# Optimization experiments

Measured on AMD Instinct MI355X. Metric: run time of the kernel, lower is better.

The kernel has to match this reference:

```python
import jax, jax.numpy as jnp
import numpy as np

B, CIN, H, W = 8, 64, 128, 128
COUT, K = 64, 3
STRIDE, PAD, DIL, G = 1, 1, 1, 1
T = K * K
HO = (H + 2 * PAD - (DIL * (K - 1) + 1)) // STRIDE + 1
WO = (W + 2 * PAD - (DIL * (K - 1) + 1)) // STRIDE + 1


def setup_inputs() -> dict:
    key = jax.random.key(0)
    ks = jax.random.split(key, 5)
    x = jax.random.normal(ks[0], (B, CIN, H, W), jnp.float32)
    offset = jax.random.normal(ks[1], (B, 2 * G * T, HO, WO), jnp.float32)
    mask = jax.random.uniform(ks[2], (B, G * T, HO, WO), jnp.float32)
    weight = jax.random.normal(ks[3], (COUT, CIN, K, K), jnp.float32) * (1.0 / np.sqrt(CIN * T))
    bias = jnp.zeros((COUT,), jnp.float32)
    return {"x": x, "offset": offset, "mask": mask, "weight": weight, "bias": bias}


def _gather(img_f, idx):
    # img_f: [Cg, H*W], idx: [T, Ho, Wo] -> [Cg, T, Ho, Wo]
    return img_f[:, idx]


def _dcn(x, offset, mask, weight, bias):
    Bn, Cin, Hh, Ww = x.shape
    Cout = weight.shape[0]
    Cg = Cin // G
    # offset channels laid out as [G, T, (dy, dx)] per DCNv2 convention
    off = offset.reshape(Bn, G, T, 2, HO, WO)
    dy, dx = off[:, :, :, 0], off[:, :, :, 1]  # [B, G, T, Ho, Wo]
    ky, kx = jnp.meshgrid(jnp.arange(K), jnp.arange(K), indexing="ij")
    ky = (ky.reshape(T) * DIL).astype(jnp.float32)
    kx = (kx.reshape(T) * DIL).astype(jnp.float32)
    base_y = (jnp.arange(HO) * STRIDE - PAD).astype(jnp.float32)
    base_x = (jnp.arange(WO) * STRIDE - PAD).astype(jnp.float32)
    # absolute sampling coordinates per (batch, def-group, tap, out-row, out-col)
    py = dy + base_y[None, None, None, :, None] + ky[None, None, :, None, None]
    px = dx + base_x[None, None, None, None, :] + kx[None, None, :, None, None]
    y0 = jnp.floor(py)
    x0 = jnp.floor(px)
    imgf = x.reshape(Bn, G, Cg, Hh * Ww)
    gather = jax.vmap(jax.vmap(_gather))  # over B and G
    sampled = jnp.zeros((Bn, G, Cg, T, HO, WO), x.dtype)
    # bilinear interpolation with zero padding outside the image
    for oy, ox in ((y0, x0), (y0, x0 + 1.0), (y0 + 1.0, x0), (y0 + 1.0, x0 + 1.0)):
        wgt = (1.0 - jnp.abs(py - oy)) * (1.0 - jnp.abs(px - ox))
        valid = (oy >= 0) & (oy < Hh) & (ox >= 0) & (ox < Ww)
        yi = jnp.clip(oy, 0, Hh - 1).astype(jnp.int32)
        xi = jnp.clip(ox, 0, Ww - 1).astype(jnp.int32)
        vals = gather(imgf, yi * Ww + xi)  # [B, G, Cg, T, Ho, Wo]
        sampled = sampled + vals * (wgt * valid)[:, :, None]
    # modulation mask, then accumulate taps into output channels
    m = mask.reshape(Bn, G, T, HO, WO)
    sampled = sampled * m[:, :, None]
    wr = weight.reshape(Cout, G, Cg, T)
    out = jnp.einsum("bgctij,ogct->boij", sampled, wr) + bias[None, :, None, None]
    return out


def reference(x, offset, mask, weight, bias):
    return _dcn(x, offset, mask, weight, bias)
```

## Files before the change

### kernel.cpp

```cpp
#include <hip/hip_runtime.h>
#include <stdint.h>

#define Bn   8
#define CIN  64
#define Hh   128
#define Wh   128
#define COUT 64
#define Tt   9
#define HO   128
#define WO   128
#define HW   (HO * WO)

#define RH     17
#define RWC    24
#define RREC   (RH * RWC)
#define HALO_Y 4
#define HALO_X 4

typedef _Float16 h16;
typedef __attribute__((ext_vector_type(2)))  _Float16 h2;
typedef __attribute__((ext_vector_type(8)))  _Float16 h8;
typedef __attribute__((ext_vector_type(16))) float    f16v;

__device__ h16 g_xT[(size_t)Bn * Hh * Wh * CIN];
__device__ h16 g_wh[Tt * 4 * 2 * 64 * 8];

__global__ __launch_bounds__(256) void prep(const float* __restrict__ x,
                                            const float* __restrict__ w) {
    if (blockIdx.x >= Bn * Hh) {
        int tid = (blockIdx.x - Bn * Hh) * 256 + threadIdx.x;
        int t   = tid >> 12;
        int rem = tid & 4095;
        int ks  = rem >> 10;
        int mt  = (rem >> 9) & 1;
        int ln  = (rem >> 3) & 63;
        int j   = rem & 7;
        int o   = mt * 32 + (ln & 31);
        int c   = ks * 16 + ((ln >> 5) << 3) + j;
        g_wh[tid] = (h16)w[(size_t)(o * 64 + c) * 9 + t];
        return;
    }
    int b = blockIdx.x >> 7;
    int y = blockIdx.x & 127;
    __shared__ uint32_t tile[64][65];

    const float* src = x + ((size_t)b * CIN) * (Hh * Wh) + (size_t)y * Wh;
    int t    = threadIdx.x;
    int xp   = t & 63;
    int csub = t >> 6;
    #pragma unroll
    for (int cc = 0; cc < 64; cc += 4) {
        int c = cc + csub;
        float2 v = *(const float2*)(src + (size_t)c * (Hh * Wh) + xp * 2);
        uint32_t h0 = (uint32_t)__builtin_bit_cast(uint16_t, (h16)v.x);
        uint32_t h1 = (uint32_t)__builtin_bit_cast(uint16_t, (h16)v.y);
        tile[c][xp] = h0 | (h1 << 16);
    }
    __syncthreads();

    uint32_t* dst = (uint32_t*)(g_xT + (((size_t)b * Hh + y) * Wh) * CIN);
    int d  = t & 31;
    int xo = t >> 5;
    #pragma unroll
    for (int it = 0; it < 16; ++it) {
        int xg = it * 8 + xo;
        uint32_t lo = tile[2 * d][xg >> 1];
        uint32_t hi = tile[2 * d + 1][xg >> 1];
        int sh = (xg & 1) * 16;
        uint32_t l0 = (lo >> sh) & 0xffffu;
        uint32_t h1 = (hi >> sh) & 0xffffu;
        dst[xg * 32 + d] = l0 | (h1 << 16);
    }
}

__global__ __launch_bounds__(256, 3) void dcn_main(
        const float* __restrict__ offset, const float* __restrict__ mask,
        const float* __restrict__ bias, float* __restrict__ out) {
    __shared__ __align__(16) uint8_t sreg[RREC * 128];

    int blk  = blockIdx.x;
    int b    = blk & 7;
    int s    = blk >> 3;
    int ty   = s >> 3, tx = s & 7;
    int i0   = ty * 8, j0 = tx * 16;
    int lane = threadIdx.x & 63;
    int wave = threadIdx.x >> 6;
    int n    = lane & 31;
    int g    = lane >> 5;

    const h16* xb = g_xT + (size_t)b * (Hh * Wh * CIN);

    int i = i0 + 2 * wave + (n >> 4);
    int j = j0 + (n & 15);
    int p = (i << 7) + j;

    const float* offB = offset + (size_t)b * (2 * Tt * HW);
    const float* mskB = mask   + (size_t)b * (Tt * HW);
    float dyv[Tt], dxv[Tt], mmv[Tt];
    #pragma unroll
    for (int t = 0; t < Tt; ++t) {
        dyv[t] = offB[(2 * t) * HW + p];
        dxv[t] = offB[(2 * t + 1) * HW + p];
        mmv[t] = mskB[t * HW + p];
    }

    {
        const int base_y = i0 - HALO_Y, base_x = j0 - HALO_X;
        #pragma unroll
        for (int it = 0; it < 13; ++it) {
            int idx  = it * 256 + threadIdx.x;
            int rec  = idx >> 3;
            int quad = idx & 7;
            if (rec < RREC) {
                int ry = rec / RWC, rx = rec - ry * RWC;
                int gy = min(max(base_y + ry, 0), Hh - 1);
                int gx = min(max(base_x + rx, 0), Wh - 1);
                uint4 v = *(const uint4*)(xb + ((gy << 7) + gx) * 64 + quad * 8);
                int qs = quad ^ (rec & 7);
                *(uint4*)(sreg + rec * 128 + qs * 16) = v;
            }
        }
    }
    __syncthreads();

    f16v acc[2] = {};

    #pragma unroll
    for (int t = 0; t < Tt; ++t) {
        const int ky = t / 3, kx = t % 3;
        float py = dyv[t] + (float)(i + ky - 1);
        float px = dxv[t] + (float)(j + kx - 1);
        float fy = floorf(py), fx = floorf(px);
        int   y0 = (int)fy,    x0 = (int)fx;
        float ly = py - fy,    lx = px - fx;
        float hy = 1.f - ly,   hx = 1.f - lx;

        bool vy0 = (y0 >= 0) && (y0 < Hh);
        bool vy1 = (y0 >= -1) && (y0 < Hh - 1);
        bool vx0 = (x0 >= 0) && (x0 < Wh);
        bool vx1 = (x0 >= -1) && (x0 < Wh - 1);
        float m = mmv[t];
        float w00 = (vy0 && vx0) ? hy * hx * m : 0.f;
        float w01 = (vy0 && vx1) ? hy * lx * m : 0.f;
        float w10 = (vy1 && vx0) ? ly * hx * m : 0.f;
        float w11 = (vy1 && vx1) ? ly * lx * m : 0.f;

        int ry = y0 - i0 + HALO_Y;
        int rx = x0 - j0 + HALO_X;
        bool intile = (ry >= 0) & (ry <= RH - 2) & (rx >= 0) & (rx <= RWC - 2);
        int ryc = min(max(ry, 0), RH - 2), rxc = min(max(rx, 0), RWC - 2);
        int pl00 = ryc * RWC + rxc;
        int r00 = pl00, r01 = pl00 + 1, r10 = pl00 + RWC, r11 = pl00 + RWC + 1;
        int q00 = ((r00 << 7) | (g << 4)) ^ ((r00 & 7) << 4);
        int q01 = ((r01 << 7) | (g << 4)) ^ ((r01 & 7) << 4);
        int q10 = ((r10 << 7) | (g << 4)) ^ ((r10 & 7) << 4);
        int q11 = ((r11 << 7) | (g << 4)) ^ ((r11 & 7) << 4);

        union U4 { uint4 v; h2 h[4]; };
        U4 c00[4], c01[4], c10[4], c11[4];
        #pragma unroll
        for (int ks = 0; ks < 4; ++ks) {
            c00[ks].v = *(const uint4*)(sreg + (q00 ^ (ks << 5)));
            c01[ks].v = *(const uint4*)(sreg + (q01 ^ (ks << 5)));
            c10[ks].v = *(const uint4*)(sreg + (q10 ^ (ks << 5)));
            c11[ks].v = *(const uint4*)(sreg + (q11 ^ (ks << 5)));
        }
        if (__any(!intile)) {
            if (!intile) {
                int y0c = min(max(y0, 0), Hh - 1), y1c = min(max(y0 + 1, 0), Hh - 1);
                int x0c = min(max(x0, 0), Wh - 1), x1c = min(max(x0 + 1, 0), Wh - 1);
                const h16* r0p = xb + (size_t)(y0c * Wh) * CIN;
                const h16* r1p = xb + (size_t)(y1c * Wh) * CIN;
                #pragma unroll
                for (int ks = 0; ks < 4; ++ks) {
                    int c = ks * 16 + g * 8;
                    c00[ks].v = *(const uint4*)(r0p + x0c * CIN + c);
                    c01[ks].v = *(const uint4*)(r0p + x1c * CIN + c);
                    c10[ks].v = *(const uint4*)(r1p + x0c * CIN + c);
                    c11[ks].v = *(const uint4*)(r1p + x1c * CIN + c);
                }
            }
        }

        h2 W00 = {(h16)w00, (h16)w00};
        h2 W01 = {(h16)w01, (h16)w01};
        h2 W10 = {(h16)w10, (h16)w10};
        h2 W11 = {(h16)w11, (h16)w11};

        const h16* wt = g_wh + t * 4096;
        #pragma unroll
        for (int ks = 0; ks < 4; ++ks) {
            union { h2 r[4]; h8 v; } pk;
            #pragma unroll
            for (int e = 0; e < 4; ++e) {
                h2 r = c00[ks].h[e] * W00;
                r = c01[ks].h[e] * W01 + r;
                r = c10[ks].h[e] * W10 + r;
                r = c11[ks].h[e] * W11 + r;
                pk.r[e] = r;
            }
            #pragma unroll
            for (int mt = 0; mt < 2; ++mt) {
                h8 a = *(const h8*)(wt + (ks * 2 + mt) * 512 + lane * 8);
                acc[mt] = __builtin_amdgcn_mfma_f32_32x32x16_f16(
                    a, pk.v, acc[mt], 0, 0, 0);
            }
        }
    }

    #pragma unroll
    for (int mt = 0; mt < 2; ++mt) {
        #pragma unroll
        for (int r = 0; r < 16; ++r) {
            int o = mt * 32 + (r & 3) + 8 * (r >> 2) + 4 * g;
            out[(size_t)(b * COUT + o) * HW + p] = acc[mt][r] + bias[o];
        }
    }
}

extern "C" void kernel_launch(void* const* d_in, const int* in_sizes, int n_in,
                              void* d_out, int out_size, void* d_ws, size_t ws_size,
                              hipStream_t stream) {
    const float* x      = (const float*)d_in[0];
    const float* offset = (const float*)d_in[1];
    const float* mask   = (const float*)d_in[2];
    const float* weight = (const float*)d_in[3];
    const float* bias   = (const float*)d_in[4];
    (void)d_ws; (void)ws_size;

    prep<<<Bn * Hh + 144, 256, 0, stream>>>(x, weight);
    dcn_main<<<Bn * 128, 256, 0, stream>>>(offset, mask, bias, (float*)d_out);
}
```

Baseline: 120.9 us.

## Process two tiles per block, prefetching second tile's halo into registers during compute

Measured after the change: 140.1 us. 15.9% more time.

```diff
diff --git a/kernel.cpp b/kernel.cpp
--- a/kernel.cpp
+++ b/kernel.cpp
@@ -73,56 +73,55 @@
     }
 }
 
-__global__ __launch_bounds__(256, 3) void dcn_main(
-        const float* __restrict__ offset, const float* __restrict__ mask,
-        const float* __restrict__ bias, float* __restrict__ out) {
-    __shared__ __align__(16) uint8_t sreg[RREC * 128];
-
-    int blk  = blockIdx.x;
-    int b    = blk & 7;
-    int s    = blk >> 3;
-    int ty   = s >> 3, tx = s & 7;
-    int i0   = ty * 8, j0 = tx * 16;
-    int lane = threadIdx.x & 63;
-    int wave = threadIdx.x >> 6;
-    int n    = lane & 31;
-    int g    = lane >> 5;
-
-    const h16* xb = g_xT + (size_t)b * (Hh * Wh * CIN);
-
-    int i = i0 + 2 * wave + (n >> 4);
-    int j = j0 + (n & 15);
-    int p = (i << 7) + j;
-
-    const float* offB = offset + (size_t)b * (2 * Tt * HW);
-    const float* mskB = mask   + (size_t)b * (Tt * HW);
-    float dyv[Tt], dxv[Tt], mmv[Tt];
+
+__device__ __forceinline__ void stage_load(const h16* __restrict__ xb,
+                                           int base_y, int base_x, int tid,
+                                           uint4 sv[13]) {
+    #pragma unroll
+    for (int it = 0; it < 13; ++it) {
+        int idx  = it * 256 + tid;
+        int rec  = idx >> 3;
+        int quad = idx & 7;
+        if (rec < RREC) {
+            int ry = rec / RWC, rx = rec - ry * RWC;
+            int gy = min(max(base_y + ry, 0), Hh - 1);
+            int gx = min(max(base_x + rx, 0), Wh - 1);
+            sv[it] = *(const uint4*)(xb + ((gy << 7) + gx) * 64 + quad * 8);
+        }
+    }
+}
+
+__device__ __forceinline__ void stage_write(uint8_t* __restrict__ sreg,
+                                            int tid, const uint4 sv[13]) {
+    #pragma unroll
+    for (int it = 0; it < 13; ++it) {
+        int idx  = it * 256 + tid;
+        int rec  = idx >> 3;
+        int quad = idx & 7;
+        if (rec < RREC) {
+            int qs = quad ^ (rec & 7);
+            *(uint4*)(sreg + rec * 128 + qs * 16) = sv[it];
+        }
+    }
+}
+
+__device__ __forceinline__ void load_offs(const float* __restrict__ offB,
+                                          const float* __restrict__ mskB,
+                                          int p, float dyv[Tt], float dxv[Tt],
+                                          float mmv[Tt]) {
     #pragma unroll
     for (int t = 0; t < Tt; ++t) {
         dyv[t] = offB[(2 * t) * HW + p];
         dxv[t] = offB[(2 * t + 1) * HW + p];
         mmv[t] = mskB[t * HW + p];
     }
-
-    {
-        const int base_y = i0 - HALO_Y, base_x = j0 - HALO_X;
-        #pragma unroll
-        for (int it = 0; it < 13; ++it) {
-            int idx  = it * 256 + threadIdx.x;
-            int rec  = idx >> 3;
-            int quad = idx & 7;
-            if (rec < RREC) {
-                int ry = rec / RWC, rx = rec - ry * RWC;
-                int gy = min(max(base_y + ry, 0), Hh - 1);
-                int gx = min(max(base_x + rx, 0), Wh - 1);
-                uint4 v = *(const uint4*)(xb + ((gy << 7) + gx) * 64 + quad * 8);
-                int qs = quad ^ (rec & 7);
-                *(uint4*)(sreg + rec * 128 + qs * 16) = v;
-            }
-        }
-    }
-    __syncthreads();
-
+}
+
+__device__ __forceinline__ void compute_tile(
+        const uint8_t* __restrict__ sreg, const h16* __restrict__ xb,
+        const float dyv[Tt], const float dxv[Tt], const float mmv[Tt],
+        int i, int j, int p, int i0, int j0, int g, int lane,
+        float* __restrict__ out, int b, const float* __restrict__ bias) {
     f16v acc[2] = {};
 
     #pragma unroll
@@ -218,6 +217,57 @@
     }
 }
 
+__global__ __launch_bounds__(256, 2) void dcn_main(
+        const float* __restrict__ offset, const float* __restrict__ mask,
+        const float* __restrict__ bias, float* __restrict__ out) {
+    __shared__ __align__(16) uint8_t sreg[RREC * 128];
+
+    int blk  = blockIdx.x;
+    int b    = blk & 7;
+    int k    = blk >> 3;
+    int ty   = k >> 2;
+    int txp  = k & 3;
+    int i0   = ty * 8;
+    int j0A  = (txp * 2) * 16;
+    int j0B  = j0A + 16;
+    int tid  = threadIdx.x;
+    int lane = tid & 63;
+    int wave = tid >> 6;
+    int n    = lane & 31;
+    int g    = lane >> 5;
+
+    const h16* xb = g_xT + (size_t)b * (Hh * Wh * CIN);
+
+    int i  = i0 + 2 * wave + (n >> 4);
+    int jA = j0A + (n & 15);
+    int pA = (i << 7) + jA;
+
+    const float* offB = offset + (size_t)b * (2 * Tt * HW);
+    const float* mskB = mask   + (size_t)b * (Tt * HW);
+
+    float dyA[Tt], dxA[Tt], mmA[Tt];
+    load_offs(offB, mskB, pA, dyA, dxA, mmA);
+
+    uint4 sv[13];
+    stage_load(xb, i0 - HALO_Y, j0A - HALO_X, tid, sv);
+    stage_write(sreg, tid, sv);
+    __syncthreads();
+
+    stage_load(xb, i0 - HALO_Y, j0B - HALO_X, tid, sv);
+    float dyB[Tt], dxB[Tt], mmB[Tt];
+    load_offs(offB, mskB, pA + 16, dyB, dxB, mmB);
+
+    compute_tile(sreg, xb, dyA, dxA, mmA, i, jA, pA, i0, j0A, g, lane,
+                 out, b, bias);
+    __syncthreads();
+
+    stage_write(sreg, tid, sv);
+    __syncthreads();
+
+    compute_tile(sreg, xb, dyB, dxB, mmB, i, jA + 16, pA + 16, i0, j0B, g,
+                 lane, out, b, bias);
+}
+
 extern "C" void kernel_launch(void* const* d_in, const int* in_sizes, int n_in,
                               void* d_out, int out_size, void* d_ws, size_t ws_size,
                               hipStream_t stream) {
@@ -229,5 +279,5 @@
     (void)d_ws; (void)ws_size;
 
     prep<<<Bn * Hh + 144, 256, 0, stream>>>(x, weight);
-    dcn_main<<<Bn * 128, 256, 0, stream>>>(offset, mask, bias, (float*)d_out);
-}
+    dcn_main<<<Bn * 64, 256, 0, stream>>>(offset, mask, bias, (float*)d_out);
+}
```
